# Kernel optimization log

Measured on AMD Instinct MI355X. Metric: run time of the kernel, lower is better.

The kernel has to match this reference:

```python
import jax, jax.numpy as jnp
import numpy as np

N_NODES = 50000

def gcn_conv(x, src, dst, W, b, n_nodes):
    # PyG GCNConv: add self-loops, symmetric normalization D^-1/2 (A+I) D^-1/2, then bias
    loop = jnp.arange(n_nodes)
    s = jnp.concatenate([src, loop])
    d = jnp.concatenate([dst, loop])
    deg = jax.ops.segment_sum(jnp.ones(s.shape[0], x.dtype), d, num_segments=n_nodes)
    dinv = jnp.where(deg > 0, jax.lax.rsqrt(deg), 0.0)
    norm = dinv[s] * dinv[d]                      # [E+N]
    h = x @ W                                      # [N, out]
    msg = h[s] * norm[:, None]                     # gather + scale
    out = jax.ops.segment_sum(msg, d, num_segments=n_nodes)  # scatter-add
    return out + b

def setup_inputs() -> dict:
    key = jax.random.key(0)
    ks = jax.random.split(key, 8)
    x = jax.random.normal(ks[0], (N_NODES, 128), jnp.float32)
    edge_index = jax.random.randint(ks[1], (2, 800000), 0, N_NODES)
    def glorot(k, fan_in, fan_out):
        lim = np.sqrt(6.0 / (fan_in + fan_out)).astype(np.float32)
        return jax.random.uniform(k, (fan_in, fan_out), jnp.float32, -lim, lim)
    return {
        "x": x,
        "edge_index": edge_index,
        "conv_w1": glorot(ks[2], 128, 64), "conv_b1": jnp.zeros((64,), jnp.float32),
        "conv_w2": glorot(ks[3], 64, 64),  "conv_b2": jnp.zeros((64,), jnp.float32),
        "fc_w1": glorot(ks[4], 64, 32),    "fc_b1": jnp.zeros((32,), jnp.float32),
        "fc_w2": glorot(ks[5], 32, 1),     "fc_b2": jnp.zeros((1,), jnp.float32),
    }

def reference(x, edge_index, conv_w1, conv_b1, conv_w2, conv_b2, fc_w1, fc_b1, fc_w2, fc_b2):
    src, dst = edge_index[0], edge_index[1]
    h = jnp.tanh(gcn_conv(x, src, dst, conv_w1, conv_b1, N_NODES))
    h = jnp.tanh(gcn_conv(h, src, dst, conv_w2, conv_b2, N_NODES))
    h = jnp.tanh(h @ fc_w1 + fc_b1)  # dropout is identity at inference
    return h @ fc_w2 + fc_b2          # [N, 1]
```

## Files before the change

kernel.cpp:

```cpp
#include <hip/hip_runtime.h>
#include <math.h>

#define TPB 256
#define NBK_MAX 512
#define CAP 4096
#define FILL_CAP 4096
#define SC_CH 16
#define DMAX 64

typedef short bf16x8 __attribute__((ext_vector_type(8)));
typedef float f32x4 __attribute__((ext_vector_type(4)));

__device__ __forceinline__ unsigned short rne_bf16(float f) {
  unsigned u = __float_as_uint(f);
  return (unsigned short)((u + 0x7fffu + ((u >> 16) & 1u)) >> 16);
}
__device__ __forceinline__ float bf16_f(unsigned short v) {
  return __uint_as_float((unsigned)v << 16);
}
__device__ __forceinline__ float blo(unsigned u) { return __uint_as_float(u << 16); }
__device__ __forceinline__ float bhi(unsigned u) { return __uint_as_float(u & 0xffff0000u); }
__device__ __forceinline__ float ftanh(float x) {
  float xc = fminf(fmaxf(x, -15.f), 15.f);
  float e = __expf(2.f * xc);
  return (e - 1.f) * __builtin_amdgcn_rcpf(e + 1.f);
}

__global__ __launch_bounds__(TPB) void k_init(int* __restrict__ gcur,
                                              unsigned short* __restrict__ hz,
                                              int NBK, int N) {
  int i = blockIdx.x * TPB + threadIdx.x;
  if (i < NBK) gcur[i] = i * CAP;
  if (blockIdx.x == 0 && threadIdx.x < 32)
    ((unsigned*)(hz + ((size_t)N << 6)))[threadIdx.x] = 0;
}

__global__ __launch_bounds__(TPB) void k_bscatter(const int* __restrict__ src,
                                                  const int* __restrict__ dst,
                                                  int* __restrict__ gcur,
                                                  unsigned* __restrict__ e2,
                                                  int E, int NBK) {
  __shared__ int h[NBK_MAX];
  __shared__ int base[NBK_MAX];
  int tid = threadIdx.x, blk = blockIdx.x, G = gridDim.x;
  int chunk = (E + G - 1) / G, lo = blk * chunk, hi = min(E, lo + chunk);
  for (int t0 = lo; t0 < hi; t0 += TPB * SC_CH) {
    int sv[SC_CH], dv[SC_CH];
    for (int b = tid; b < NBK; b += TPB) h[b] = 0;
    __syncthreads();
#pragma unroll
    for (int u = 0; u < SC_CH; ++u) {
      int e = t0 + u * TPB + tid;
      if (e < hi) {
        dv[u] = dst[e];
        sv[u] = src[e];
        atomicAdd(&h[dv[u] >> 7], 1);
      } else {
        dv[u] = -1;
      }
    }
    __syncthreads();
    for (int b = tid; b < NBK; b += TPB) {
      int c = h[b];
      if (c) {
        int o = atomicAdd(&gcur[b], c);
        base[b] = min(o, (b + 1) * CAP - c);
      }
    }
    __syncthreads();
    for (int b = tid; b < NBK; b += TPB) h[b] = 0;
    __syncthreads();
#pragma unroll
    for (int u = 0; u < SC_CH; ++u) {
      if (dv[u] >= 0) {
        int bk = dv[u] >> 7;
        int r = atomicAdd(&h[bk], 1);
        e2[base[bk] + r] = ((unsigned)sv[u] << 7) | (unsigned)(dv[u] & 127);
      }
    }
    __syncthreads();
  }
}

__global__ __launch_bounds__(TPB) void k_build(const unsigned* __restrict__ e2,
                                               const int* __restrict__ gcur,
                                               float* __restrict__ dinv,
                                               int* __restrict__ col2, int N) {
  __shared__ int c[128], sc[128], cur[128];
  __shared__ int buf[FILL_CAP];
  int tid = threadIdx.x, b = blockIdx.x;
  int st = b * CAP;
  int en = min(gcur[b], st + FILL_CAP);
  if (tid < 128) c[tid] = 0;
  __syncthreads();
  for (int i = st + tid; i < en; i += TPB) atomicAdd(&c[e2[i] & 127u], 1);
  __syncthreads();
  if (tid < 128) sc[tid] = c[tid];
  __syncthreads();
  for (int o = 1; o < 128; o <<= 1) {
    int v = (tid >= o && tid < 128) ? sc[tid - o] : 0;
    __syncthreads();
    if (tid < 128) sc[tid] += v;
    __syncthreads();
  }
  if (tid < 128) {
    cur[tid] = sc[tid] - c[tid];
    int node = b * 128 + tid;
    if (node < N) dinv[node] = rsqrtf((float)(c[tid] + 1));
  }
  __syncthreads();
  for (int i = st + tid; i < en; i += TPB) {
    unsigned v = e2[i];
    int p = atomicAdd(&cur[v & 127u], 1);
    buf[p] = (int)(v >> 7);
  }
  __syncthreads();
  for (int i = tid; i < 128 * DMAX; i += TPB) {
    int nl = i >> 6, k = i & 63;
    int node = b * 128 + nl;
    if (node < N) {
      int cc = c[nl];
      col2[((size_t)node << 6) + k] = (k < cc) ? buf[sc[nl] - cc + k] : N;
    }
  }
}

template <int K, bool AF32>
__global__ __launch_bounds__(TPB) void k_mm(const void* __restrict__ Ap,
                                            const float* __restrict__ W,
                                            const float* __restrict__ dinv,
                                            unsigned short* __restrict__ Hout, int N) {
  constexpr int P = K + 8;
  __shared__ unsigned short sHi[64 * P];
  __shared__ unsigned short sLo[64 * P];
  int tid = threadIdx.x;
  for (int i = tid; i < K * 64; i += TPB) {
    int k = i >> 6, n = i & 63;
    float w = W[i];
    unsigned short hb = rne_bf16(w);
    sHi[n * P + k] = hb;
    sLo[n * P + k] = rne_bf16(w - bf16_f(hb));
  }
  __syncthreads();
  int wave = tid >> 6, lane = tid & 63;
  int oct = lane >> 4, l15 = lane & 15;
  int base = blockIdx.x * 64 + wave * 16;
  int arow = base + l15;
  if (arow >= N) arow = N - 1;
  f32x4 acc[4] = {};
#pragma unroll
  for (int s = 0; s < K / 32; ++s) {
    bf16x8 ahi, alo;
    if (AF32) {
      const float* ap = (const float*)Ap + (size_t)arow * K + s * 32 + oct * 8;
      float4 f0 = *(const float4*)ap;
      float4 f1 = *(const float4*)(ap + 4);
      float fv[8] = {f0.x, f0.y, f0.z, f0.w, f1.x, f1.y, f1.z, f1.w};
#pragma unroll
      for (int j = 0; j < 8; ++j) {
        unsigned short hb = rne_bf16(fv[j]);
        ahi[j] = (short)hb;
        alo[j] = (short)rne_bf16(fv[j] - bf16_f(hb));
      }
    } else {
      ahi = *(const bf16x8*)((const unsigned short*)Ap + (size_t)arow * K + s * 32 + oct * 8);
    }
#pragma unroll
    for (int t = 0; t < 4; ++t) {
      bf16x8 bh = *(const bf16x8*)(sHi + (t * 16 + l15) * P + s * 32 + oct * 8);
      bf16x8 bl = *(const bf16x8*)(sLo + (t * 16 + l15) * P + s * 32 + oct * 8);
      acc[t] = __builtin_amdgcn_mfma_f32_16x16x32_bf16(ahi, bh, acc[t], 0, 0, 0);
      acc[t] = __builtin_amdgcn_mfma_f32_16x16x32_bf16(ahi, bl, acc[t], 0, 0, 0);
      if (AF32)
        acc[t] = __builtin_amdgcn_mfma_f32_16x16x32_bf16(alo, bh, acc[t], 0, 0, 0);
    }
  }
#pragma unroll
  for (int r = 0; r < 4; ++r) {
    int row = base + oct * 4 + r;
    if (row < N) {
      float dv = dinv[row];
#pragma unroll
      for (int t = 0; t < 4; ++t)
        Hout[(size_t)row * 64 + t * 16 + l15] = rne_bf16(acc[t][r] * dv);
    }
  }
}


#define AQ_ISSUE(J, HVS)                                                        \
  {                                                                             \
    unsigned long long mb_ = __ballot(sv[J] != NS);                             \
    cnt[J] = __builtin_amdgcn_readfirstlane((int)__popcll(mb_));                \
    _Pragma("unroll") for (int g = 0; g < 8; ++g) {                             \
      int s0 = __builtin_amdgcn_readlane(sv[J], g);                             \
      int s1 = __builtin_amdgcn_readlane(sv[J], 8 + g);                         \
      int s = half ? s1 : s0;                                                   \
      HVS[0][g] = *(const unsigned*)(H + ((size_t)s << 6) + f2 * 2);            \
    }                                                                           \
    if (cnt[J] > 16) {                                                          \
      _Pragma("unroll") for (int g = 0; g < 8; ++g) {                           \
        int s0 = __builtin_amdgcn_readlane(sv[J], 16 + g);                      \
        int s1 = __builtin_amdgcn_readlane(sv[J], 24 + g);                      \
        int s = half ? s1 : s0;                                                 \
        HVS[1][g] = *(const unsigned*)(H + ((size_t)s << 6) + f2 * 2);          \
      }                                                                         \
    }                                                                           \
  }

#define AQ_ACC(J, HVS)                                                          \
  {                                                                             \
    float x = (half == 0) ? blo(sf[J]) : 0.f;                                   \
    float y = (half == 0) ? bhi(sf[J]) : 0.f;                                   \
    _Pragma("unroll") for (int g = 0; g < 8; ++g) {                             \
      x += blo(HVS[0][g]);                                                      \
      y += bhi(HVS[0][g]);                                                      \
    }                                                                           \
    if (cnt[J] > 16) {                                                          \
      _Pragma("unroll") for (int g = 0; g < 8; ++g) {                           \
        x += blo(HVS[1][g]);                                                    \
        y += bhi(HVS[1][g]);                                                    \
      }                                                                         \
    }                                                                           \
    for (int t = 32; t < cnt[J]; t += 16) {         \
      unsigned tv[8];                                                           \
      _Pragma("unroll") for (int g = 0; g < 8; ++g) {                           \
        int s0 = __builtin_amdgcn_readlane(sv[J], t + g);                       \
        int s1 = __builtin_amdgcn_readlane(sv[J], t + 8 + g);                   \
        int s = half ? s1 : s0;                                                 \
        tv[g] = *(const unsigned*)(H + ((size_t)s << 6) + f2 * 2);              \
      }                                                                         \
      _Pragma("unroll") for (int g = 0; g < 8; ++g) {                           \
        x += blo(tv[g]);                                                        \
        y += bhi(tv[g]);                                                        \
      }                                                                         \
    }                                                                           \
    x += __shfl_xor(x, 32);                                                     \
    y += __shfl_xor(y, 32);                                                     \
    ax[J] = x;                                                                  \
    ay[J] = y;                                                                  \
  }

__device__ __forceinline__ void agg_quad(int i0, int NS,
                                         const unsigned short* __restrict__ H,
                                         const int* __restrict__ col2,
                                         float* ax, float* ay) {
  int lane = threadIdx.x & 63;
  int f2 = lane & 31, half = lane >> 5;
  int idx[4];
#pragma unroll
  for (int j = 0; j < 4; ++j) idx[j] = min(i0 + j, NS - 1);
  int sv[4];
  unsigned sf[4];
#pragma unroll
  for (int j = 0; j < 4; ++j) sv[j] = col2[((size_t)idx[j] << 6) + lane];
#pragma unroll
  for (int j = 0; j < 4; ++j)
    sf[j] = *(const unsigned*)(H + ((size_t)idx[j] << 6) + f2 * 2);
  unsigned hvA[2][8], hvB[2][8];
  int cnt[4];
  AQ_ISSUE(0, hvA)
  AQ_ISSUE(1, hvB)
  AQ_ACC(0, hvA)
  AQ_ISSUE(2, hvA)
  AQ_ACC(1, hvB)
  AQ_ISSUE(3, hvB)
  AQ_ACC(2, hvA)
  AQ_ACC(3, hvB)
}

template <bool DOFC>
__global__ __launch_bounds__(TPB) void k_agg(const unsigned short* __restrict__ H,
                                             const int* __restrict__ col2,
                                             const float* __restrict__ dinv,
                                             const float* __restrict__ bias,
                                             unsigned short* __restrict__ OUT,
                                             const float* __restrict__ fw1,
                                             const float* __restrict__ fb1,
                                             const float* __restrict__ fw2,
                                             const float* __restrict__ fb2,
                                             float* __restrict__ fout, int N) {
  int tid = threadIdx.x;
  int wid = tid >> 6, lane = tid & 63;
  int f2 = lane & 31, half = lane >> 5;
  float2 bf = *(const float2*)(bias + f2 * 2);
  if constexpr (!DOFC) {
    int qb = blockIdx.x * 16 + wid * 4;
    if (qb >= N) return;
    float dv[4];
#pragma unroll
    for (int j = 0; j < 4; ++j) dv[j] = dinv[min(qb + j, N - 1)];
    float ax[4], ay[4];
    agg_quad(qb, N, H, col2, ax, ay);
    if (half == 0) {
#pragma unroll
      for (int j = 0; j < 4; ++j) {
        int node = qb + j;
        if (node < N) {
          unsigned pk = (unsigned)rne_bf16(ftanh(dv[j] * ax[j] + bf.x)) |
                        ((unsigned)rne_bf16(ftanh(dv[j] * ay[j] + bf.y)) << 16);
          ((unsigned*)OUT)[((size_t)node << 5) + f2] = pk;
        }
      }
    }
  } else {
    __shared__ float sw1t[32 * 66];
    __shared__ float sb1[32];
    __shared__ float sw2[32];
    __shared__ float sA[16 * 64];
    for (int i = tid; i < 32 * 64; i += TPB) {
      int j = i >> 6, k = i & 63;
      sw1t[j * 66 + k] = fw1[k * 32 + j];
    }
    if (tid < 32) { sb1[tid] = fb1[tid]; sw2[tid] = fw2[tid]; }
    __syncthreads();
    int ngroups = (N + 15) / 16;
    float b2v = fb2[0];
    for (int grp = blockIdx.x; grp < ngroups; grp += gridDim.x) {
      int qb = grp * 16 + wid * 4;
      float dv[4];
#pragma unroll
      for (int j = 0; j < 4; ++j) dv[j] = dinv[min(qb + j, N - 1)];
      float ax[4], ay[4];
      agg_quad(qb, N, H, col2, ax, ay);
      if (half == 0) {
#pragma unroll
        for (int j = 0; j < 4; ++j) {
          int nl = wid * 4 + j;
          sA[nl * 64 + f2 * 2 + 0] = ftanh(dv[j] * ax[j] + bf.x);
          sA[nl * 64 + f2 * 2 + 1] = ftanh(dv[j] * ay[j] + bf.y);
        }
      }
      __syncthreads();
#pragma unroll
      for (int hg = 0; hg < 2; ++hg) {
        int nl = (tid >> 5) + hg * 8;
        int j = tid & 31;
        int node = grp * 16 + nl;
        if (node < N) {
          float acc = sb1[j];
          const float2* ar = (const float2*)(sA + nl * 64);
          const float2* wr = (const float2*)(sw1t + j * 66);
#pragma unroll
          for (int k2 = 0; k2 < 32; ++k2) {
            float2 av = ar[k2];
            float2 wv = wr[k2];
            acc += av.x * wv.x + av.y * wv.y;
          }
          float t = ftanh(acc) * sw2[j];
#pragma unroll
          for (int o = 1; o < 32; o <<= 1) t += __shfl_xor(t, o);
          if (j == 0) fout[node] = t + b2v;
        }
      }
      __syncthreads();
    }
  }
}


extern "C" void kernel_launch(void* const* d_in, const int* in_sizes, int n_in,
                              void* d_out, int out_size, void* d_ws, size_t ws_size,
                              hipStream_t stream) {
  const float* x   = (const float*)d_in[0];
  const int*   ei  = (const int*)d_in[1];
  const float* w1  = (const float*)d_in[2];
  const float* b1  = (const float*)d_in[3];
  const float* w2  = (const float*)d_in[4];
  const float* b2  = (const float*)d_in[5];
  const float* fw1 = (const float*)d_in[6];
  const float* fb1 = (const float*)d_in[7];
  const float* fw2 = (const float*)d_in[8];
  const float* fb2 = (const float*)d_in[9];
  float* out = (float*)d_out;

  int N = in_sizes[0] / 128;
  int E = in_sizes[1] / 2;
  const int* src = ei;
  const int* dst = ei + E;

  const int G   = 256;
  const int NBK = (N + 127) / 128;

  char* p = (char*)d_ws;
  size_t off = 0;
  auto take = [&](size_t bytes) -> void* {
    void* r = p + off;
    off += (bytes + 255) & ~(size_t)255;
    return r;
  };
  int*            gcur = (int*)take((size_t)NBK * 4);
  float*          dinv = (float*)take((size_t)N * 4);
  unsigned*       e2   = (unsigned*)take((size_t)NBK * CAP * 4);
  int*            col2 = (int*)take((size_t)N * DMAX * 4);
  unsigned short* h    = (unsigned short*)take((size_t)(N + 1) * 64 * 2);
  unsigned short* a    = (unsigned short*)take((size_t)N * 64 * 2);
  (void)ws_size; (void)n_in; (void)out_size;

  k_init<<<(NBK + TPB - 1) / TPB, TPB, 0, stream>>>(gcur, h, NBK, N);
  k_bscatter<<<G, TPB, 0, stream>>>(src, dst, gcur, e2, E, NBK);
  k_build<<<NBK, TPB, 0, stream>>>(e2, gcur, dinv, col2, N);

  int gmm = (N + 63) / 64;
  int gagg = (N + 15) / 16;
  k_mm<128, true><<<gmm, TPB, 0, stream>>>(x, w1, dinv, h, N);
  k_agg<false><<<gagg, TPB, 0, stream>>>(h, col2, dinv, b1, a,
                                         nullptr, nullptr, nullptr, nullptr,
                                         nullptr, N);
  k_mm<64, false><<<gmm, TPB, 0, stream>>>(a, w2, dinv, h, N);
  k_agg<true><<<gagg, TPB, 0, stream>>>(h, col2, dinv, b2, nullptr,
                                        fw1, fb1, fw2, fb2, out, N);
}
```

Before: 182.4 us.

## Restructure GCN aggregation with 16-byte row gathers and self-loop in adjacency

Aggregation now has each lane load a 16-byte chunk of a neighbor's bf16 row, so eight lanes cover one row and eight neighbors are gathered per instruction. Lane-sum reductions over shuffles replace the old per-4-byte gathers. The self-loop is stored as the first entry of each adjacency row, and dinv is recomputed from the neighbor count, which removes the separate self-row and dinv loads. Each warp now handles 8 nodes with a software-pipelined issue/accumulate schedule, and the FC epilogue drops its block-level barriers and grid-stride loop. This adds shuffle-reduction work and register pressure, and nodes with 64 or more in-edges now lose one extra neighbor because the self-loop takes a slot.

```diff
diff --git a/kernel.cpp b/kernel.cpp
--- a/kernel.cpp
+++ b/kernel.cpp
@@ -120,7 +120,11 @@
     int node = b * 128 + nl;
     if (node < N) {
       int cc = c[nl];
-      col2[((size_t)node << 6) + k] = (k < cc) ? buf[sc[nl] - cc + k] : N;
+      int v;
+      if (k == 0) v = node;
+      else if (k - 1 < cc) v = buf[sc[nl] - cc + k - 1];
+      else v = N;
+      col2[((size_t)node << 6) + k] = v;
     }
   }
 }
@@ -188,91 +192,74 @@
 }
 
 
-#define AQ_ISSUE(J, HVS)                                                        \
+__device__ __forceinline__ uint4 ldrow(const unsigned short* __restrict__ H, int s, int f8) {
+  return *(const uint4*)(H + ((size_t)s << 6) + f8 * 8);
+}
+__device__ __forceinline__ void unp(uint4 u, float* a) {
+  a[0] += blo(u.x); a[1] += bhi(u.x);
+  a[2] += blo(u.y); a[3] += bhi(u.y);
+  a[4] += blo(u.z); a[5] += bhi(u.z);
+  a[6] += blo(u.w); a[7] += bhi(u.w);
+}
+
+#define GISS(B, J)                                                              \
   {                                                                             \
-    unsigned long long mb_ = __ballot(sv[J] != NS);                             \
-    cnt[J] = __builtin_amdgcn_readfirstlane((int)__popcll(mb_));                \
-    _Pragma("unroll") for (int g = 0; g < 8; ++g) {                             \
-      int s0 = __builtin_amdgcn_readlane(sv[J], g);                             \
-      int s1 = __builtin_amdgcn_readlane(sv[J], 8 + g);                         \
-      int s = half ? s1 : s0;                                                   \
-      HVS[0][g] = *(const unsigned*)(H + ((size_t)s << 6) + f2 * 2);            \
-    }                                                                           \
-    if (cnt[J] > 16) {                                                          \
-      _Pragma("unroll") for (int g = 0; g < 8; ++g) {                           \
-        int s0 = __builtin_amdgcn_readlane(sv[J], 16 + g);                      \
-        int s1 = __builtin_amdgcn_readlane(sv[J], 24 + g);                      \
-        int s = half ? s1 : s0;                                                 \
-        HVS[1][g] = *(const unsigned*)(H + ((size_t)s << 6) + f2 * 2);          \
+    int s0_ = __shfl(sv[J], e8);                                                \
+    int s1_ = __shfl(sv[J], 8 + e8);                                            \
+    int s2_ = __shfl(sv[J], 16 + e8);                                           \
+    int s3_ = __shfl(sv[J], 24 + e8);                                           \
+    B[0] = ldrow(H, s0_, f8);                                                   \
+    B[1] = ldrow(H, s1_, f8);                                                   \
+    B[2] = ldrow(H, s2_, f8);                                                   \
+    B[3] = ldrow(H, s3_, f8);                                                   \
+  }
+
+#define GACC(B, J)                                                              \
+  {                                                                             \
+    float ac[8] = {0.f, 0.f, 0.f, 0.f, 0.f, 0.f, 0.f, 0.f};                     \
+    unp(B[0], ac); unp(B[1], ac); unp(B[2], ac); unp(B[3], ac);                 \
+    if (cnt[J] > 32) {                                     \
+      for (int t = 32; t < cnt[J]; t += 16) {                                   \
+        int sx_ = __shfl(sv[J], t + e8);                                        \
+        int sy_ = __shfl(sv[J], t + 8 + e8);                                    \
+        uint4 ex_ = ldrow(H, sx_, f8);                                          \
+        uint4 ey_ = ldrow(H, sy_, f8);                                          \
+        unp(ex_, ac); unp(ey_, ac);                                             \
       }                                                                         \
     }                                                                           \
-  }
-
-#define AQ_ACC(J, HVS)                                                          \
-  {                                                                             \
-    float x = (half == 0) ? blo(sf[J]) : 0.f;                                   \
-    float y = (half == 0) ? bhi(sf[J]) : 0.f;                                   \
-    _Pragma("unroll") for (int g = 0; g < 8; ++g) {                             \
-      x += blo(HVS[0][g]);                                                      \
-      y += bhi(HVS[0][g]);                                                      \
+    _Pragma("unroll") for (int r = 0; r < 8; ++r) {                             \
+      ac[r] += __shfl_xor(ac[r], 8);                                            \
+      ac[r] += __shfl_xor(ac[r], 16);                                           \
+      ac[r] += __shfl_xor(ac[r], 32);                                           \
     }                                                                           \
-    if (cnt[J] > 16) {                                                          \
-      _Pragma("unroll") for (int g = 0; g < 8; ++g) {                           \
-        x += blo(HVS[1][g]);                                                    \
-        y += bhi(HVS[1][g]);                                                    \
+    if (e8 == 0) {                                                              \
+      float di_ = rsqrtf((float)cnt[J]);                                        \
+      float y0 = ftanh(di_ * ac[0] + bb[0]);                                    \
+      float y1 = ftanh(di_ * ac[1] + bb[1]);                                    \
+      float y2 = ftanh(di_ * ac[2] + bb[2]);                                    \
+      float y3 = ftanh(di_ * ac[3] + bb[3]);                                    \
+      float y4 = ftanh(di_ * ac[4] + bb[4]);                                    \
+      float y5 = ftanh(di_ * ac[5] + bb[5]);                                    \
+      float y6 = ftanh(di_ * ac[6] + bb[6]);                                    \
+      float y7 = ftanh(di_ * ac[7] + bb[7]);                                    \
+      if constexpr (DOFC) {                                                     \
+        float* sp_ = sA + ((wid << 3) + (J)) * 64 + f8 * 8;                     \
+        *(float4*)sp_ = make_float4(y0, y1, y2, y3);                            \
+        *(float4*)(sp_ + 4) = make_float4(y4, y5, y6, y7);                      \
+      } else {                                                                  \
+        uint4 pk_;                                                              \
+        pk_.x = (unsigned)rne_bf16(y0) | ((unsigned)rne_bf16(y1) << 16);        \
+        pk_.y = (unsigned)rne_bf16(y2) | ((unsigned)rne_bf16(y3) << 16);        \
+        pk_.z = (unsigned)rne_bf16(y4) | ((unsigned)rne_bf16(y5) << 16);        \
+        pk_.w = (unsigned)rne_bf16(y6) | ((unsigned)rne_bf16(y7) << 16);        \
+        *((uint4*)OUT + ((size_t)idx[J] << 3) + f8) = pk_;                      \
       }                                                                         \
     }                                                                           \
-    for (int t = 32; t < cnt[J]; t += 16) {         \
-      unsigned tv[8];                                                           \
-      _Pragma("unroll") for (int g = 0; g < 8; ++g) {                           \
-        int s0 = __builtin_amdgcn_readlane(sv[J], t + g);                       \
-        int s1 = __builtin_amdgcn_readlane(sv[J], t + 8 + g);                   \
-        int s = half ? s1 : s0;                                                 \
-        tv[g] = *(const unsigned*)(H + ((size_t)s << 6) + f2 * 2);              \
-      }                                                                         \
-      _Pragma("unroll") for (int g = 0; g < 8; ++g) {                           \
-        x += blo(tv[g]);                                                        \
-        y += bhi(tv[g]);                                                        \
-      }                                                                         \
-    }                                                                           \
-    x += __shfl_xor(x, 32);                                                     \
-    y += __shfl_xor(y, 32);                                                     \
-    ax[J] = x;                                                                  \
-    ay[J] = y;                                                                  \
-  }
-
-__device__ __forceinline__ void agg_quad(int i0, int NS,
-                                         const unsigned short* __restrict__ H,
-                                         const int* __restrict__ col2,
-                                         float* ax, float* ay) {
-  int lane = threadIdx.x & 63;
-  int f2 = lane & 31, half = lane >> 5;
-  int idx[4];
-#pragma unroll
-  for (int j = 0; j < 4; ++j) idx[j] = min(i0 + j, NS - 1);
-  int sv[4];
-  unsigned sf[4];
-#pragma unroll
-  for (int j = 0; j < 4; ++j) sv[j] = col2[((size_t)idx[j] << 6) + lane];
-#pragma unroll
-  for (int j = 0; j < 4; ++j)
-    sf[j] = *(const unsigned*)(H + ((size_t)idx[j] << 6) + f2 * 2);
-  unsigned hvA[2][8], hvB[2][8];
-  int cnt[4];
-  AQ_ISSUE(0, hvA)
-  AQ_ISSUE(1, hvB)
-  AQ_ACC(0, hvA)
-  AQ_ISSUE(2, hvA)
-  AQ_ACC(1, hvB)
-  AQ_ISSUE(3, hvB)
-  AQ_ACC(2, hvA)
-  AQ_ACC(3, hvB)
-}
+  }
 
 template <bool DOFC>
 __global__ __launch_bounds__(TPB) void k_agg(const unsigned short* __restrict__ H,
                                              const int* __restrict__ col2,
-                                             const float* __restrict__ dinv,
                                              const float* __restrict__ bias,
                                              unsigned short* __restrict__ OUT,
                                              const float* __restrict__ fw1,
@@ -280,80 +267,80 @@
                                              const float* __restrict__ fw2,
                                              const float* __restrict__ fb2,
                                              float* __restrict__ fout, int N) {
+  __shared__ float sw1t[32 * 66];
+  __shared__ float sb1[32];
+  __shared__ float sw2[32];
+  __shared__ float sA[4 * 8 * 64];
   int tid = threadIdx.x;
   int wid = tid >> 6, lane = tid & 63;
-  int f2 = lane & 31, half = lane >> 5;
-  float2 bf = *(const float2*)(bias + f2 * 2);
-  if constexpr (!DOFC) {
-    int qb = blockIdx.x * 16 + wid * 4;
-    if (qb >= N) return;
-    float dv[4];
-#pragma unroll
-    for (int j = 0; j < 4; ++j) dv[j] = dinv[min(qb + j, N - 1)];
-    float ax[4], ay[4];
-    agg_quad(qb, N, H, col2, ax, ay);
-    if (half == 0) {
-#pragma unroll
-      for (int j = 0; j < 4; ++j) {
-        int node = qb + j;
-        if (node < N) {
-          unsigned pk = (unsigned)rne_bf16(ftanh(dv[j] * ax[j] + bf.x)) |
-                        ((unsigned)rne_bf16(ftanh(dv[j] * ay[j] + bf.y)) << 16);
-          ((unsigned*)OUT)[((size_t)node << 5) + f2] = pk;
-        }
-      }
-    }
-  } else {
-    __shared__ float sw1t[32 * 66];
-    __shared__ float sb1[32];
-    __shared__ float sw2[32];
-    __shared__ float sA[16 * 64];
+  int e8 = lane >> 3, f8 = lane & 7;
+  float b2v = 0.f;
+  if constexpr (DOFC) {
     for (int i = tid; i < 32 * 64; i += TPB) {
       int j = i >> 6, k = i & 63;
       sw1t[j * 66 + k] = fw1[k * 32 + j];
     }
     if (tid < 32) { sb1[tid] = fb1[tid]; sw2[tid] = fw2[tid]; }
-    __syncthreads();
-    int ngroups = (N + 15) / 16;
-    float b2v = fb2[0];
-    for (int grp = blockIdx.x; grp < ngroups; grp += gridDim.x) {
-      int qb = grp * 16 + wid * 4;
-      float dv[4];
-#pragma unroll
-      for (int j = 0; j < 4; ++j) dv[j] = dinv[min(qb + j, N - 1)];
-      float ax[4], ay[4];
-      agg_quad(qb, N, H, col2, ax, ay);
-      if (half == 0) {
-#pragma unroll
-        for (int j = 0; j < 4; ++j) {
-          int nl = wid * 4 + j;
-          sA[nl * 64 + f2 * 2 + 0] = ftanh(dv[j] * ax[j] + bf.x);
-          sA[nl * 64 + f2 * 2 + 1] = ftanh(dv[j] * ay[j] + bf.y);
-        }
+    b2v = fb2[0];
+    __syncthreads();
+  }
+  float4 bb0 = *(const float4*)(bias + f8 * 8);
+  float4 bb1 = *(const float4*)(bias + f8 * 8 + 4);
+  float bb[8] = {bb0.x, bb0.y, bb0.z, bb0.w, bb1.x, bb1.y, bb1.z, bb1.w};
+
+  int qb = (blockIdx.x * 4 + wid) * 8;
+  if constexpr (!DOFC) {
+    if (qb >= N) return;
+  }
+  int idx[8];
+#pragma unroll
+  for (int j = 0; j < 8; ++j) idx[j] = min(qb + j, N - 1);
+  int sv[8];
+#pragma unroll
+  for (int j = 0; j < 8; ++j) sv[j] = col2[((size_t)idx[j] << 6) + lane];
+  int cnt[8];
+#pragma unroll
+  for (int j = 0; j < 8; ++j) {
+    unsigned long long mb_ = __ballot(sv[j] != N);
+    cnt[j] = __builtin_amdgcn_readfirstlane((int)__popcll(mb_));
+  }
+  uint4 bufA[4], bufB[4];
+  GISS(bufA, 0)
+  GISS(bufB, 1)
+  GACC(bufA, 0)
+  GISS(bufA, 2)
+  GACC(bufB, 1)
+  GISS(bufB, 3)
+  GACC(bufA, 2)
+  GISS(bufA, 4)
+  GACC(bufB, 3)
+  GISS(bufB, 5)
+  GACC(bufA, 4)
+  GISS(bufA, 6)
+  GACC(bufB, 5)
+  GISS(bufB, 7)
+  GACC(bufA, 6)
+  GACC(bufB, 7)
+
+  if constexpr (DOFC) {
+    int half = lane >> 5, m = lane & 31;
+#pragma unroll
+    for (int p = 0; p < 4; ++p) {
+      int nl = p * 2 + half;
+      int node = qb + nl;
+      float acc = sb1[m];
+      const float2* ar = (const float2*)(sA + ((wid << 3) + nl) * 64);
+      const float2* wr = (const float2*)(sw1t + m * 66);
+#pragma unroll
+      for (int k2 = 0; k2 < 32; ++k2) {
+        float2 av = ar[k2];
+        float2 wv = wr[k2];
+        acc += av.x * wv.x + av.y * wv.y;
       }
-      __syncthreads();
-#pragma unroll
-      for (int hg = 0; hg < 2; ++hg) {
-        int nl = (tid >> 5) + hg * 8;
-        int j = tid & 31;
-        int node = grp * 16 + nl;
-        if (node < N) {
-          float acc = sb1[j];
-          const float2* ar = (const float2*)(sA + nl * 64);
-          const float2* wr = (const float2*)(sw1t + j * 66);
-#pragma unroll
-          for (int k2 = 0; k2 < 32; ++k2) {
-            float2 av = ar[k2];
-            float2 wv = wr[k2];
-            acc += av.x * wv.x + av.y * wv.y;
-          }
-          float t = ftanh(acc) * sw2[j];
-#pragma unroll
-          for (int o = 1; o < 32; o <<= 1) t += __shfl_xor(t, o);
-          if (j == 0) fout[node] = t + b2v;
-        }
-      }
-      __syncthreads();
+      float t = ftanh(acc) * sw2[m];
+#pragma unroll
+      for (int o = 1; o < 32; o <<= 1) t += __shfl_xor(t, o);
+      if (m == 0 && node < N) fout[node] = t + b2v;
     }
   }
 }
@@ -402,12 +389,12 @@
   k_build<<<NBK, TPB, 0, stream>>>(e2, gcur, dinv, col2, N);
 
   int gmm = (N + 63) / 64;
-  int gagg = (N + 15) / 16;
+  int gagg = (N + 31) / 32;
   k_mm<128, true><<<gmm, TPB, 0, stream>>>(x, w1, dinv, h, N);
-  k_agg<false><<<gagg, TPB, 0, stream>>>(h, col2, dinv, b1, a,
+  k_agg<false><<<gagg, TPB, 0, stream>>>(h, col2, b1, a,
                                          nullptr, nullptr, nullptr, nullptr,
                                          nullptr, N);
   k_mm<64, false><<<gmm, TPB, 0, stream>>>(a, w2, dinv, h, N);
-  k_agg<true><<<gagg, TPB, 0, stream>>>(h, col2, dinv, b2, nullptr,
+  k_agg<true><<<gagg, TPB, 0, stream>>>(h, col2, b2, nullptr,
                                         fw1, fb1, fw2, fb2, out, N);
 }
```

Result: slower. 197.3 us (+8.1%).

## Store self-loop in adjacency and process eight nodes per wave in aggregation

Applied to the files above, without the earlier changes.

The adjacency table now stores each node's self-loop as entry zero, so the separate self-feature load is gone, and the destination degree normalization is recomputed from the neighbour count with rsqrt instead of loaded from dinv. The aggregation kernel handles eight nodes per wave instead of four, with all counts computed up front and a deeper software-pipelined gather sequence. The FC head is reorganized per wave without block-wide barriers and without the grid-stride loop. The risks are higher register pressure and a neighbour table that can hold one fewer real neighbour per node.

```diff
diff --git a/kernel.cpp b/kernel.cpp
--- a/kernel.cpp
+++ b/kernel.cpp
@@ -120,7 +120,11 @@
     int node = b * 128 + nl;
     if (node < N) {
       int cc = c[nl];
-      col2[((size_t)node << 6) + k] = (k < cc) ? buf[sc[nl] - cc + k] : N;
+      int v;
+      if (k == 0) v = node;
+      else if (k - 1 < cc) v = buf[sc[nl] - cc + k - 1];
+      else v = N;
+      col2[((size_t)node << 6) + k] = v;
     }
   }
 }
@@ -190,8 +194,6 @@
 
 #define AQ_ISSUE(J, HVS)                                                        \
   {                                                                             \
-    unsigned long long mb_ = __ballot(sv[J] != NS);                             \
-    cnt[J] = __builtin_amdgcn_readfirstlane((int)__popcll(mb_));                \
     _Pragma("unroll") for (int g = 0; g < 8; ++g) {                             \
       int s0 = __builtin_amdgcn_readlane(sv[J], g);                             \
       int s1 = __builtin_amdgcn_readlane(sv[J], 8 + g);                         \
@@ -210,8 +212,7 @@
 
 #define AQ_ACC(J, HVS)                                                          \
   {                                                                             \
-    float x = (half == 0) ? blo(sf[J]) : 0.f;                                   \
-    float y = (half == 0) ? bhi(sf[J]) : 0.f;                                   \
+    float x = 0.f, y = 0.f;                                                     \
     _Pragma("unroll") for (int g = 0; g < 8; ++g) {                             \
       x += blo(HVS[0][g]);                                                      \
       y += bhi(HVS[0][g]);                                                      \
@@ -221,44 +222,84 @@
         x += blo(HVS[1][g]);                                                    \
         y += bhi(HVS[1][g]);                                                    \
       }                                                                         \
-    }                                                                           \
-    for (int t = 32; t < cnt[J]; t += 16) {         \
-      unsigned tv[8];                                                           \
-      _Pragma("unroll") for (int g = 0; g < 8; ++g) {                           \
-        int s0 = __builtin_amdgcn_readlane(sv[J], t + g);                       \
-        int s1 = __builtin_amdgcn_readlane(sv[J], t + 8 + g);                   \
-        int s = half ? s1 : s0;                                                 \
-        tv[g] = *(const unsigned*)(H + ((size_t)s << 6) + f2 * 2);              \
-      }                                                                         \
-      _Pragma("unroll") for (int g = 0; g < 8; ++g) {                           \
-        x += blo(tv[g]);                                                        \
-        y += bhi(tv[g]);                                                        \
+      for (int t = 32; t < cnt[J]; t += 16) {              \
+        unsigned tv[8];                                                         \
+        _Pragma("unroll") for (int g = 0; g < 8; ++g) {                         \
+          int s0 = __builtin_amdgcn_readlane(sv[J], t + g);                     \
+          int s1 = __builtin_amdgcn_readlane(sv[J], t + 8 + g);                 \
+          int s = half ? s1 : s0;                                               \
+          tv[g] = *(const unsigned*)(H + ((size_t)s << 6) + f2 * 2);            \
+        }                                                                       \
+        _Pragma("unroll") for (int g = 0; g < 8; ++g) {                         \
+          x += blo(tv[g]);                                                      \
+          y += bhi(tv[g]);                                                      \
+        }                                                                       \
       }                                                                         \
     }                                                                           \
     x += __shfl_xor(x, 32);                                                     \
     y += __shfl_xor(y, 32);                                                     \
-    ax[J] = x;                                                                  \
-    ay[J] = y;                                                                  \
-  }
-
-__device__ __forceinline__ void agg_quad(int i0, int NS,
-                                         const unsigned short* __restrict__ H,
-                                         const int* __restrict__ col2,
-                                         float* ax, float* ay) {
-  int lane = threadIdx.x & 63;
+    float di_ = rsqrtf((float)cnt[J]);                                          \
+    float yx_ = ftanh(di_ * x + bf.x);                                          \
+    float yy_ = ftanh(di_ * y + bf.y);                                          \
+    if constexpr (DOFC) {                                                       \
+      if (half == 0) {                                                          \
+        float* sp_ = sA + ((wid << 3) + (J)) * 64 + f2 * 2;                     \
+        sp_[0] = yx_;                                                           \
+        sp_[1] = yy_;                                                           \
+      }                                                                         \
+    } else {                                                                    \
+      if (half == 0 && qb + (J) < N) {                                          \
+        unsigned pk_ = (unsigned)rne_bf16(yx_) | ((unsigned)rne_bf16(yy_) << 16); \
+        ((unsigned*)OUT)[((size_t)(qb + (J)) << 5) + f2] = pk_;                 \
+      }                                                                         \
+    }                                                                           \
+  }
+
+template <bool DOFC>
+__global__ __launch_bounds__(TPB) void k_agg(const unsigned short* __restrict__ H,
+                                             const int* __restrict__ col2,
+                                             const float* __restrict__ bias,
+                                             unsigned short* __restrict__ OUT,
+                                             const float* __restrict__ fw1,
+                                             const float* __restrict__ fb1,
+                                             const float* __restrict__ fw2,
+                                             const float* __restrict__ fb2,
+                                             float* __restrict__ fout, int N) {
+  __shared__ float sw1t[DOFC ? 32 * 66 : 1];
+  __shared__ float sb1[DOFC ? 32 : 1];
+  __shared__ float sw2[DOFC ? 32 : 1];
+  __shared__ float sA[DOFC ? 4 * 8 * 64 : 1];
+  int tid = threadIdx.x;
+  int wid = tid >> 6, lane = tid & 63;
   int f2 = lane & 31, half = lane >> 5;
-  int idx[4];
-#pragma unroll
-  for (int j = 0; j < 4; ++j) idx[j] = min(i0 + j, NS - 1);
-  int sv[4];
-  unsigned sf[4];
-#pragma unroll
-  for (int j = 0; j < 4; ++j) sv[j] = col2[((size_t)idx[j] << 6) + lane];
-#pragma unroll
-  for (int j = 0; j < 4; ++j)
-    sf[j] = *(const unsigned*)(H + ((size_t)idx[j] << 6) + f2 * 2);
+  float b2v = 0.f;
+  if constexpr (DOFC) {
+    for (int i = tid; i < 32 * 64; i += TPB) {
+      int j = i >> 6, k = i & 63;
+      sw1t[j * 66 + k] = fw1[k * 32 + j];
+    }
+    if (tid < 32) { sb1[tid] = fb1[tid]; sw2[tid] = fw2[tid]; }
+    b2v = fb2[0];
+    __syncthreads();
+  }
+  float2 bf = *(const float2*)(bias + f2 * 2);
+
+  int qb = (blockIdx.x * 4 + wid) * 8;
+  if (qb >= N) return;
+
+  int idx[8];
+#pragma unroll
+  for (int j = 0; j < 8; ++j) idx[j] = min(qb + j, N - 1);
+  int sv[8];
+#pragma unroll
+  for (int j = 0; j < 8; ++j) sv[j] = col2[((size_t)idx[j] << 6) + lane];
+  int cnt[8];
+#pragma unroll
+  for (int j = 0; j < 8; ++j) {
+    unsigned long long mb_ = __ballot(sv[j] != N);
+    cnt[j] = __builtin_amdgcn_readfirstlane((int)__popcll(mb_));
+  }
   unsigned hvA[2][8], hvB[2][8];
-  int cnt[4];
   AQ_ISSUE(0, hvA)
   AQ_ISSUE(1, hvB)
   AQ_ACC(0, hvA)
@@ -266,94 +307,35 @@
   AQ_ACC(1, hvB)
   AQ_ISSUE(3, hvB)
   AQ_ACC(2, hvA)
+  AQ_ISSUE(4, hvA)
   AQ_ACC(3, hvB)
-}
-
-template <bool DOFC>
-__global__ __launch_bounds__(TPB) void k_agg(const unsigned short* __restrict__ H,
-                                             const int* __restrict__ col2,
-                                             const float* __restrict__ dinv,
-                                             const float* __restrict__ bias,
-                                             unsigned short* __restrict__ OUT,
-                                             const float* __restrict__ fw1,
-                                             const float* __restrict__ fb1,
-                                             const float* __restrict__ fw2,
-                                             const float* __restrict__ fb2,
-                                             float* __restrict__ fout, int N) {
-  int tid = threadIdx.x;
-  int wid = tid >> 6, lane = tid & 63;
-  int f2 = lane & 31, half = lane >> 5;
-  float2 bf = *(const float2*)(bias + f2 * 2);
-  if constexpr (!DOFC) {
-    int qb = blockIdx.x * 16 + wid * 4;
-    if (qb >= N) return;
-    float dv[4];
-#pragma unroll
-    for (int j = 0; j < 4; ++j) dv[j] = dinv[min(qb + j, N - 1)];
-    float ax[4], ay[4];
-    agg_quad(qb, N, H, col2, ax, ay);
-    if (half == 0) {
-#pragma unroll
-      for (int j = 0; j < 4; ++j) {
-        int node = qb + j;
-        if (node < N) {
-          unsigned pk = (unsigned)rne_bf16(ftanh(dv[j] * ax[j] + bf.x)) |
-                        ((unsigned)rne_bf16(ftanh(dv[j] * ay[j] + bf.y)) << 16);
-          ((unsigned*)OUT)[((size_t)node << 5) + f2] = pk;
-        }
-      }
-    }
-  } else {
-    __shared__ float sw1t[32 * 66];
-    __shared__ float sb1[32];
-    __shared__ float sw2[32];
-    __shared__ float sA[16 * 64];
-    for (int i = tid; i < 32 * 64; i += TPB) {
-      int j = i >> 6, k = i & 63;
-      sw1t[j * 66 + k] = fw1[k * 32 + j];
-    }
-    if (tid < 32) { sb1[tid] = fb1[tid]; sw2[tid] = fw2[tid]; }
-    __syncthreads();
-    int ngroups = (N + 15) / 16;
-    float b2v = fb2[0];
-    for (int grp = blockIdx.x; grp < ngroups; grp += gridDim.x) {
-      int qb = grp * 16 + wid * 4;
-      float dv[4];
-#pragma unroll
-      for (int j = 0; j < 4; ++j) dv[j] = dinv[min(qb + j, N - 1)];
-      float ax[4], ay[4];
-      agg_quad(qb, N, H, col2, ax, ay);
-      if (half == 0) {
-#pragma unroll
-        for (int j = 0; j < 4; ++j) {
-          int nl = wid * 4 + j;
-          sA[nl * 64 + f2 * 2 + 0] = ftanh(dv[j] * ax[j] + bf.x);
-          sA[nl * 64 + f2 * 2 + 1] = ftanh(dv[j] * ay[j] + bf.y);
-        }
-      }
-      __syncthreads();
-#pragma unroll
-      for (int hg = 0; hg < 2; ++hg) {
-        int nl = (tid >> 5) + hg * 8;
-        int j = tid & 31;
-        int node = grp * 16 + nl;
-        if (node < N) {
-          float acc = sb1[j];
-          const float2* ar = (const float2*)(sA + nl * 64);
-          const float2* wr = (const float2*)(sw1t + j * 66);
-#pragma unroll
-          for (int k2 = 0; k2 < 32; ++k2) {
-            float2 av = ar[k2];
-            float2 wv = wr[k2];
-            acc += av.x * wv.x + av.y * wv.y;
-          }
-          float t = ftanh(acc) * sw2[j];
-#pragma unroll
-          for (int o = 1; o < 32; o <<= 1) t += __shfl_xor(t, o);
-          if (j == 0) fout[node] = t + b2v;
-        }
-      }
-      __syncthreads();
+  AQ_ISSUE(5, hvB)
+  AQ_ACC(4, hvA)
+  AQ_ISSUE(6, hvA)
+  AQ_ACC(5, hvB)
+  AQ_ISSUE(7, hvB)
+  AQ_ACC(6, hvA)
+  AQ_ACC(7, hvB)
+
+  if constexpr (DOFC) {
+    int m = lane & 31;
+#pragma unroll
+    for (int p = 0; p < 4; ++p) {
+      int nl = p * 2 + half;
+      int node = qb + nl;
+      float acc = sb1[m];
+      const float2* ar = (const float2*)(sA + ((wid << 3) + nl) * 64);
+      const float2* wr = (const float2*)(sw1t + m * 66);
+#pragma unroll
+      for (int k2 = 0; k2 < 32; ++k2) {
+        float2 av = ar[k2];
+        float2 wv = wr[k2];
+        acc += av.x * wv.x + av.y * wv.y;
+      }
+      float t = ftanh(acc) * sw2[m];
+#pragma unroll
+      for (int o = 1; o < 32; o <<= 1) t += __shfl_xor(t, o);
+      if (m == 0 && node < N) fout[node] = t + b2v;
     }
   }
 }
@@ -402,12 +384,12 @@
   k_build<<<NBK, TPB, 0, stream>>>(e2, gcur, dinv, col2, N);
 
   int gmm = (N + 63) / 64;
-  int gagg = (N + 15) / 16;
+  int gagg = (N + 31) / 32;
   k_mm<128, true><<<gmm, TPB, 0, stream>>>(x, w1, dinv, h, N);
-  k_agg<false><<<gagg, TPB, 0, stream>>>(h, col2, dinv, b1, a,
+  k_agg<false><<<gagg, TPB, 0, stream>>>(h, col2, b1, a,
                                          nullptr, nullptr, nullptr, nullptr,
                                          nullptr, N);
   k_mm<64, false><<<gmm, TPB, 0, stream>>>(a, w2, dinv, h, N);
-  k_agg<true><<<gagg, TPB, 0, stream>>>(h, col2, dinv, b2, nullptr,
+  k_agg<true><<<gagg, TPB, 0, stream>>>(h, col2, b2, nullptr,
                                         fw1, fb1, fw2, fb2, out, N);
 }
```

Result: slower. 188.5 us (+3.3%).
